# Kernel tuning notes

Measured on AMD Instinct MI355X. Metric: run time of the kernel, lower is better.

The kernel has to match this reference:

```python
import jax, jax.numpy as jnp
import numpy as np

N_NODES = 100000


def gcn_conv(x, edge_index, W, b):
    """PyG GCNConv: add self-loops, symmetric deg^{-1/2} normalization,
    linear transform, scatter-add aggregation, then bias."""
    n = x.shape[0]
    loops = jnp.arange(n, dtype=edge_index.dtype)
    src = jnp.concatenate([edge_index[0], loops])  # [E+N]
    dst = jnp.concatenate([edge_index[1], loops])  # [E+N]
    # degree (with self-loops) of each target node
    deg = jax.ops.segment_sum(jnp.ones_like(dst, dtype=x.dtype), dst, num_segments=n)
    dinv = jnp.where(deg > 0, jax.lax.rsqrt(deg), 0.0)
    norm = dinv[src] * dinv[dst]  # [E+N]
    h = x @ W  # [N, out_dim] -- transform before aggregation
    msg = h[src] * norm[:, None]  # gather + normalize
    out = jax.ops.segment_sum(msg, dst, num_segments=n)  # scatter-add
    return out + b


def setup_inputs() -> dict:
    key = jax.random.key(0)
    ks = jax.random.split(key, 8)
    n, e, d_in, d_h = N_NODES, 1600000, 32, 64
    x = jax.random.normal(ks[0], (n, d_in), dtype=jnp.float32)
    edge_index = jax.random.randint(ks[1], (2, e), 0, n, dtype=jnp.int64)
    # Glorot-style init for GCN weights, uniform for linear layer
    W1 = jax.random.normal(ks[2], (d_in, d_h), dtype=jnp.float32) / np.sqrt(d_in)
    b1 = jnp.zeros((d_h,), dtype=jnp.float32)
    W2 = jax.random.normal(ks[3], (d_h, d_h), dtype=jnp.float32) / np.sqrt(d_h)
    b2 = jnp.zeros((d_h,), dtype=jnp.float32)
    Wo = jax.random.normal(ks[4], (d_h, 1), dtype=jnp.float32) / np.sqrt(d_h)
    bo = jnp.zeros((1,), dtype=jnp.float32)
    return {"x": x, "edge_index": edge_index, "W1": W1, "b1": b1,
            "W2": W2, "b2": b2, "Wo": Wo, "bo": bo}


def reference(x, edge_index, W1, b1, W2, b2, Wo, bo):
    h = jax.nn.relu(gcn_conv(x, edge_index, W1, b1))
    h = jax.nn.relu(gcn_conv(h, edge_index, W2, b2))
    logits = h @ Wo + bo  # [N, 1]
    return jax.nn.sigmoid(logits).squeeze(-1)  # [N]
```

## Files before the change

### kernel.cpp

```cpp
#include <hip/hip_runtime.h>

#define DH 64
#define DIN 32
#define BSH 8
#define BNODES 256
#define MAXB 1024
#define CAPSH 13
#define CAP (1 << CAPSH)

typedef unsigned short u16;
typedef unsigned int u32;
typedef float f32x2 __attribute__((ext_vector_type(2)));

__device__ __forceinline__ float bf2f(u16 u) {
    union { u32 i; float f; } x; x.i = ((u32)u) << 16; return x.f;
}
__device__ __forceinline__ u16 f2bf(float f) {
    union { float f; u32 i; } x; x.f = f;
    u32 r = x.i + 0x7fff + ((x.i >> 16) & 1);
    return (u16)(r >> 16);
}
__device__ __forceinline__ float bfl(u32 u) {
    union { u32 i; float f; } x; x.i = u << 16; return x.f;
}
__device__ __forceinline__ float bfh(u32 u) {
    union { u32 i; float f; } x; x.i = u & 0xffff0000u; return x.f;
}
__device__ __forceinline__ void pkacc(f32x2& a, u32 u) {
    f32x2 b;
    b[0] = bfl(u); b[1] = bfh(u);
    asm("v_pk_add_f32 %0, %1, %0" : "+v"(a) : "v"(b));
}

__global__ void __launch_bounds__(256) binA_k(
        const int* __restrict__ ei, int* __restrict__ gcnt,
        u32* __restrict__ pairs, int E, int n, int nbuck) {
    __shared__ int lhist[MAXB];
    __shared__ int lbase[MAXB];
    __shared__ int smode;
    int t = threadIdx.x;
    if (t < 64) {
        int v = (2 * t + 1 < 2 * E) ? ei[2 * t + 1] : 0;
        unsigned long long b = __ballot(v != 0);
        if (t == 0) smode = (b != 0ULL) ? 1 : 0;
    }
    for (int b = t; b < nbuck; b += 256) lhist[b] = 0;
    __syncthreads();
    int m = smode;
    unsigned un = (unsigned)n;
    int q0 = blockIdx.x * 256 + t;
    int qs = gridDim.x * 256;

    if (m && !(E & 3)) {
        const int4* d4 = (const int4*)(ei + E);
        for (int q = q0; q < (E >> 2); q += qs) {
            int4 d = d4[q];
            if ((unsigned)d.x < un) atomicAdd(&lhist[d.x >> BSH], 1);
            if ((unsigned)d.y < un) atomicAdd(&lhist[d.y >> BSH], 1);
            if ((unsigned)d.z < un) atomicAdd(&lhist[d.z >> BSH], 1);
            if ((unsigned)d.w < un) atomicAdd(&lhist[d.w >> BSH], 1);
        }
    } else if (!m && !(E & 1)) {
        const int4* d4 = (const int4*)(ei + 2 * E);
        for (int q = q0; q < (E >> 1); q += qs) {
            int4 d = d4[q];
            if ((unsigned)d.x < un) atomicAdd(&lhist[d.x >> BSH], 1);
            if ((unsigned)d.z < un) atomicAdd(&lhist[d.z >> BSH], 1);
        }
    } else {
        const int* dstp = m ? (ei + E) : (ei + 2 * E);
        int stride = m ? 1 : 2;
        for (int e = q0; e < E; e += qs) {
            int d = dstp[(size_t)e * stride];
            if ((unsigned)d < un) atomicAdd(&lhist[d >> BSH], 1);
        }
    }
    __syncthreads();
    for (int b = t; b < nbuck; b += 256) {
        int c = lhist[b];
        lbase[b] = c ? ((b << CAPSH) + atomicAdd(&gcnt[b], c)) : 0;
        lhist[b] = 0;
    }
    __syncthreads();
    #define EMIT(S, D)                                                     \
        if ((unsigned)(D) < un) {                                          \
            int sv = ((unsigned)(S) < un) ? (S) : 0;                       \
            int bb = (D) >> BSH;                                           \
            int off = atomicAdd(&lhist[bb], 1);                            \
            int pos = lbase[bb] + off;                                     \
            if (pos < ((bb + 1) << CAPSH))                                 \
                pairs[pos] = ((u32)sv << BSH) | (u32)((D) & (BNODES - 1)); \
        }
    if (m && !(E & 3)) {
        const int4* s4 = (const int4*)ei;
        const int4* d4 = (const int4*)(ei + E);
        for (int q = q0; q < (E >> 2); q += qs) {
            int4 s = s4[q]; int4 d = d4[q];
            EMIT(s.x, d.x) EMIT(s.y, d.y) EMIT(s.z, d.z) EMIT(s.w, d.w)
        }
    } else if (!m && !(E & 1)) {
        const int4* s4 = (const int4*)ei;
        const int4* d4 = (const int4*)(ei + 2 * E);
        for (int q = q0; q < (E >> 1); q += qs) {
            int4 s = s4[q]; int4 d = d4[q];
            EMIT(s.x, d.x) EMIT(s.z, d.z)
        }
    } else {
        const int* srcp = ei;
        const int* dstp = m ? (ei + E) : (ei + 2 * E);
        int stride = m ? 1 : 2;
        for (int e = q0; e < E; e += qs) {
            int d = dstp[(size_t)e * stride];
            int s = srcp[(size_t)e * stride];
            EMIT(s, d)
        }
    }
    #undef EMIT
}

__global__ void __launch_bounds__(512) csr_build_k(
        const u32* __restrict__ pairs, const int* __restrict__ gcnt,
        int* __restrict__ rstart, int* __restrict__ rend,
        int* __restrict__ col, float* __restrict__ dinv, int N) {
    __shared__ int cnt[BNODES];
    __shared__ int s[BNODES];
    int b = blockIdx.x, t = threadIdx.x;
    int base = b << CAPSH;
    int ec = gcnt[b]; if (ec > CAP) ec = CAP;
    int end = base + ec;
    if (t < BNODES) cnt[t] = 0;
    __syncthreads();
    for (int i = base + t; i < end; i += 512)
        atomicAdd(&cnt[pairs[i] & (BNODES - 1)], 1);
    __syncthreads();
    int v = (t < BNODES) ? cnt[t] : 0;
    if (t < BNODES) s[t] = v;
    __syncthreads();
    for (int off = 1; off < BNODES; off <<= 1) {
        int xsc = (t >= off && t < BNODES) ? s[t - off] : 0;
        __syncthreads();
        if (t < BNODES) s[t] += xsc;
        __syncthreads();
    }
    if (t < BNODES) {
        int excl = s[t] - v;
        int a = base + excl;
        int node = (b << BSH) + t;
        if (node < N) {
            rstart[node] = a;
            rend[node]   = a + v;
            dinv[node]   = rsqrtf((float)v + 1.0f);
        }
        cnt[t] = a;
    }
    __syncthreads();
    for (int i = base + t; i < end; i += 512) {
        u32 p = pairs[i];
        int pos = atomicAdd(&cnt[p & (BNODES - 1)], 1);
        col[pos] = (int)(p >> BSH);
    }
}

__global__ void __launch_bounds__(256) gemm1_k(
        const float* __restrict__ x, const float* __restrict__ W1,
        const float* __restrict__ dinv, u16* __restrict__ hp, int N) {
    __shared__ float Wl[DIN * DH];
    __shared__ float xl[16][DIN + 4];
    int t = threadIdx.x;
    {
        const float4* Wv = (const float4*)W1;
        float4* Wd = (float4*)Wl;
        #pragma unroll
        for (int r = 0; r < 2; r++) Wd[t + 256 * r] = Wv[t + 256 * r];
    }
    if (blockIdx.x == 0 && t < 32)
        ((float*)(hp + (size_t)N * DH))[t] = 0.f;
    if (t < 128) {
        int row = t >> 3, ck = (t & 7) * 4;
        int node = blockIdx.x * 16 + row;
        float4 vx = {0.f, 0.f, 0.f, 0.f};
        if (node < N)
            vx = *(const float4*)&x[(size_t)node * DIN + ck];
        *(float4*)&xl[row][ck] = vx;
    }
    __syncthreads();
    int lane = t & 63, w = t >> 6;
    int g = lane >> 4, c = lane & 15;
    int nl = w * 4 + g;
    int node = blockIdx.x * 16 + nl;
    const float* xr = xl[nl];
    float4 acc = {0.f, 0.f, 0.f, 0.f};
    #pragma unroll
    for (int k = 0; k < DIN; k++) {
        float xv = xr[k];
        float4 wv = *(const float4*)&Wl[k * DH + c * 4];
        acc.x += xv * wv.x; acc.y += xv * wv.y; acc.z += xv * wv.z; acc.w += xv * wv.w;
    }
    if (node < N) {
        float di = dinv[node];
        ushort4 o;
        o.x = f2bf(acc.x * di); o.y = f2bf(acc.y * di);
        o.z = f2bf(acc.z * di); o.w = f2bf(acc.w * di);
        *(ushort4*)&hp[(size_t)node * DH + c * 4] = o;
    }
}

__device__ __forceinline__ void edge_sum8_db(const u16* __restrict__ hp,
                                             const int* __restrict__ col,
                                             int start, int deg, int g, int c,
                                             int nsent, f32x2* __restrict__ acc) {
    int dm = deg;
    dm = max(dm, __shfl_xor(dm, 8, 64));
    dm = max(dm, __shfl_xor(dm, 16, 64));
    dm = max(dm, __shfl_xor(dm, 32, 64));
    if (dm <= 0) return;
    int gl = g << 3;
    u32 co = (u32)c << 4;
    const char* hpb = (const char*)hp;
    #define COLS(B) (((B) < dm && (B) + c < deg) ? col[start + (B) + c] : nsent)
    #define ISSUE(V, CB)                                                     \
        { _Pragma("unroll") for (int j = 0; j < 8; j++) {                    \
              int s_ = __shfl((CB), gl | j, 64);                             \
              (V)[j] = *(const uint4*)(hpb + ((((u32)s_) << 7) | co)); } }
    #define ACCUM(V)                                                         \
        { _Pragma("unroll") for (int j = 0; j < 8; j++) {                    \
              pkacc(acc[0], (V)[j].x); pkacc(acc[1], (V)[j].y);              \
              pkacc(acc[2], (V)[j].z); pkacc(acc[3], (V)[j].w); } }
    uint4 va[8], vb[8];
    int cbA = COLS(0);
    ISSUE(va, cbA)
    int cbB = COLS(8);
    for (int base = 0; base < dm; base += 16) {
        bool hb = base + 8 < dm;
        if (hb) ISSUE(vb, cbB)
        int cbN1 = COLS(base + 16);
        ACCUM(va)
        if (base + 16 < dm) ISSUE(va, cbN1)
        int cbN2 = COLS(base + 24);
        if (hb) ACCUM(vb)
        cbB = cbN2;
    }
    #undef COLS
    #undef ISSUE
    #undef ACCUM
}

__global__ void __launch_bounds__(256) agg_gemm_k(
        const u16* __restrict__ hp, const int* __restrict__ rstart,
        const int* __restrict__ rend, const int* __restrict__ col,
        const float* __restrict__ dinv, const float* __restrict__ b1,
        const float* __restrict__ W2, u16* __restrict__ hp2, int N) {
    __shared__ float Wl[DH * DH];
    __shared__ float xs[4][8][DH + 4];
    int tid = threadIdx.x;
    {
        const float4* Wv = (const float4*)W2;
        float4* Wd = (float4*)Wl;
        #pragma unroll
        for (int r = 0; r < 4; r++) Wd[tid + 256 * r] = Wv[tid + 256 * r];
    }
    if (blockIdx.x == 0 && tid < 32)
        ((float*)(hp2 + (size_t)N * DH))[tid] = 0.f;
    __syncthreads();
    int lane = tid & 63, w = tid >> 6;
    int g = lane >> 3, c = lane & 7;
    int node = blockIdx.x * 32 + w * 8 + g;
    int start = 0, deg = 0;
    if (node < N) { start = rstart[node]; deg = rend[node] - start; }
    f32x2 acc[4] = {{0.f,0.f},{0.f,0.f},{0.f,0.f},{0.f,0.f}};
    edge_sum8_db(hp, col, start, deg, g, c, N, acc);
    float di = (node < N) ? dinv[node] : 0.f;
    float o0=0.f,o1=0.f,o2=0.f,o3=0.f,o4=0.f,o5=0.f,o6=0.f,o7=0.f;
    if (node < N) {
        uint4 sv = *(const uint4*)&hp[(size_t)node * DH + c * 8];
        float4 blo = *(const float4*)&b1[c * 8];
        float4 bhi = *(const float4*)&b1[c * 8 + 4];
        o0 = fmaxf((acc[0][0] + bfl(sv.x)) * di + blo.x, 0.f);
        o1 = fmaxf((acc[0][1] + bfh(sv.x)) * di + blo.y, 0.f);
        o2 = fmaxf((acc[1][0] + bfl(sv.y)) * di + blo.z, 0.f);
        o3 = fmaxf((acc[1][1] + bfh(sv.y)) * di + blo.w, 0.f);
        o4 = fmaxf((acc[2][0] + bfl(sv.z)) * di + bhi.x, 0.f);
        o5 = fmaxf((acc[2][1] + bfh(sv.z)) * di + bhi.y, 0.f);
        o6 = fmaxf((acc[3][0] + bfl(sv.w)) * di + bhi.z, 0.f);
        o7 = fmaxf((acc[3][1] + bfh(sv.w)) * di + bhi.w, 0.f);
    }
    *(float4*)&xs[w][g][c * 8]     = make_float4(o0, o1, o2, o3);
    *(float4*)&xs[w][g][c * 8 + 4] = make_float4(o4, o5, o6, o7);
    const float* xr = xs[w][g];
    float4 alo = {0.f,0.f,0.f,0.f}, ahi = {0.f,0.f,0.f,0.f};
    #pragma unroll
    for (int k4 = 0; k4 < DH / 4; k4++) {
        float4 xv4 = *(const float4*)&xr[k4 * 4];
        float xj[4] = {xv4.x, xv4.y, xv4.z, xv4.w};
        #pragma unroll
        for (int j = 0; j < 4; j++) {
            const float* wr = &Wl[(k4 * 4 + j) * DH + c * 8];
            float4 w0 = *(const float4*)wr;
            float4 w1 = *(const float4*)(wr + 4);
            float xv = xj[j];
            alo.x += xv * w0.x; alo.y += xv * w0.y; alo.z += xv * w0.z; alo.w += xv * w0.w;
            ahi.x += xv * w1.x; ahi.y += xv * w1.y; ahi.z += xv * w1.z; ahi.w += xv * w1.w;
        }
    }
    if (node < N) {
        uint4 po;
        po.x = (u32)f2bf(alo.x * di) | ((u32)f2bf(alo.y * di) << 16);
        po.y = (u32)f2bf(alo.z * di) | ((u32)f2bf(alo.w * di) << 16);
        po.z = (u32)f2bf(ahi.x * di) | ((u32)f2bf(ahi.y * di) << 16);
        po.w = (u32)f2bf(ahi.z * di) | ((u32)f2bf(ahi.w * di) << 16);
        *(uint4*)&hp2[(size_t)node * DH + c * 8] = po;
    }
}

__global__ void __launch_bounds__(256) agg_head_k(
        const u16* __restrict__ hp, const int* __restrict__ rstart,
        const int* __restrict__ rend, const int* __restrict__ col,
        const float* __restrict__ dinv, const float* __restrict__ bias,
        const float* __restrict__ Wo, const float* __restrict__ bo,
        float* __restrict__ y, int N) {
    int lane = threadIdx.x & 63;
    int g = lane >> 3, c = lane & 7;
    int node = blockIdx.x * 32 + (threadIdx.x >> 6) * 8 + g;
    int start = 0, deg = 0;
    if (node < N) { start = rstart[node]; deg = rend[node] - start; }
    f32x2 acc[4] = {{0.f,0.f},{0.f,0.f},{0.f,0.f},{0.f,0.f}};
    edge_sum8_db(hp, col, start, deg, g, c, N, acc);
    float t = 0.f;
    if (node < N) {
        uint4 sv = *(const uint4*)&hp[(size_t)node * DH + c * 8];
        float4 blo = *(const float4*)&bias[c * 8];
        float4 bhi = *(const float4*)&bias[c * 8 + 4];
        float4 wlo = *(const float4*)&Wo[c * 8];
        float4 whi = *(const float4*)&Wo[c * 8 + 4];
        float di = dinv[node];
        t = fmaxf((acc[0][0] + bfl(sv.x)) * di + blo.x, 0.f) * wlo.x
          + fmaxf((acc[0][1] + bfh(sv.x)) * di + blo.y, 0.f) * wlo.y
          + fmaxf((acc[1][0] + bfl(sv.y)) * di + blo.z, 0.f) * wlo.z
          + fmaxf((acc[1][1] + bfh(sv.y)) * di + blo.w, 0.f) * wlo.w
          + fmaxf((acc[2][0] + bfl(sv.z)) * di + bhi.x, 0.f) * whi.x
          + fmaxf((acc[2][1] + bfh(sv.z)) * di + bhi.y, 0.f) * whi.y
          + fmaxf((acc[3][0] + bfl(sv.w)) * di + bhi.z, 0.f) * whi.z
          + fmaxf((acc[3][1] + bfh(sv.w)) * di + bhi.w, 0.f) * whi.w;
    }
    t += __shfl_xor(t, 1, 64);
    t += __shfl_xor(t, 2, 64);
    t += __shfl_xor(t, 4, 64);
    if (c == 0 && node < N) {
        float z = t + bo[0];
        y[node] = 1.f / (1.f + __expf(-z));
    }
}

extern "C" void kernel_launch(void* const* d_in, const int* in_sizes, int n_in,
                              void* d_out, int out_size, void* d_ws, size_t ws_size,
                              hipStream_t stream) {
    const float* x  = (const float*)d_in[0];
    const int*   ei = (const int*)d_in[1];
    const float* W1 = (const float*)d_in[2];
    const float* b1 = (const float*)d_in[3];
    const float* W2 = (const float*)d_in[4];
    const float* b2 = (const float*)d_in[5];
    const float* Wo = (const float*)d_in[6];
    const float* bo = (const float*)d_in[7];
    float* y = (float*)d_out;

    int N = in_sizes[0] / DIN;
    int E = in_sizes[1] / 2;
    int nbuck = ((N - 1) >> BSH) + 1;

    char* ws = (char*)d_ws;
    size_t off = 0;
    auto alloc = [&](size_t bytes) { char* p = ws + off; off += (bytes + 255) & ~(size_t)255; return p; };
    int*   gcnt   = (int*)alloc(MAXB * 4);
    int*   rstart = (int*)alloc((size_t)N * 4);
    int*   rend   = (int*)alloc((size_t)N * 4);
    float* dinv   = (float*)alloc((size_t)N * 4);
    int*   col    = (int*)alloc(((size_t)nbuck << CAPSH) * 4);
    size_t pair_b = ((size_t)nbuck << CAPSH) * 4;
    size_t hp_b   = (size_t)N * DH * 2 + 256;
    char*  bufA   = (char*)alloc(pair_b > hp_b ? pair_b : hp_b);
    u16*   bufB   = (u16*)alloc(hp_b);
    u16*   hp    = (u16*)bufA;
    u32*   pairs = (u32*)bufA;

    hipMemsetAsync(gcnt, 0, (size_t)nbuck * 4, stream);
    binA_k<<<256, 256, 0, stream>>>(ei, gcnt, pairs, E, N, nbuck);
    csr_build_k<<<nbuck, 512, 0, stream>>>(pairs, gcnt, rstart, rend, col, dinv, N);
    gemm1_k<<<(N + 15) / 16, 256, 0, stream>>>(x, W1, dinv, hp, N);
    agg_gemm_k<<<(N + 31) / 32, 256, 0, stream>>>(hp, rstart, rend, col, dinv, b1, W2, bufB, N);
    agg_head_k<<<(N + 31) / 32, 256, 0, stream>>>(bufB, rstart, rend, col, dinv, b2, Wo, bo, y, N);
}
```

Before: 195.6 us.

## Use rolling gather pipeline, pre-shifted column offsets, shuffle-based GEMM, larger binning blocks

The double-buffered 16-wide gather in the aggregation kernels is replaced by a rolling 8-register pipeline that overlaps each load with accumulation, which cuts register pressure. Occupancy hints of 8 blocks per CU are added. Column indices are now stored as byte offsets (index shifted left by 7), so the gather no longer shifts. The second-layer GEMM broadcasts activations with wave shuffles instead of staging them in shared memory. The binning kernel runs 512 threads per block. Smaller in-flight load depth may reduce memory-level parallelism per wave, and the shifted offsets limit node counts to what fits in 32 bits.

```diff
diff --git a/kernel.cpp b/kernel.cpp
--- a/kernel.cpp
+++ b/kernel.cpp
@@ -32,7 +32,7 @@
     asm("v_pk_add_f32 %0, %1, %0" : "+v"(a) : "v"(b));
 }
 
-__global__ void __launch_bounds__(256) binA_k(
+__global__ void __launch_bounds__(512) binA_k(
         const int* __restrict__ ei, int* __restrict__ gcnt,
         u32* __restrict__ pairs, int E, int n, int nbuck) {
     __shared__ int lhist[MAXB];
@@ -44,12 +44,12 @@
         unsigned long long b = __ballot(v != 0);
         if (t == 0) smode = (b != 0ULL) ? 1 : 0;
     }
-    for (int b = t; b < nbuck; b += 256) lhist[b] = 0;
+    for (int b = t; b < nbuck; b += 512) lhist[b] = 0;
     __syncthreads();
     int m = smode;
     unsigned un = (unsigned)n;
-    int q0 = blockIdx.x * 256 + t;
-    int qs = gridDim.x * 256;
+    int q0 = blockIdx.x * 512 + t;
+    int qs = gridDim.x * 512;
 
     if (m && !(E & 3)) {
         const int4* d4 = (const int4*)(ei + E);
@@ -76,7 +76,7 @@
         }
     }
     __syncthreads();
-    for (int b = t; b < nbuck; b += 256) {
+    for (int b = t; b < nbuck; b += 512) {
         int c = lhist[b];
         lbase[b] = c ? ((b << CAPSH) + atomicAdd(&gcnt[b], c)) : 0;
         lhist[b] = 0;
@@ -157,7 +157,7 @@
     for (int i = base + t; i < end; i += 512) {
         u32 p = pairs[i];
         int pos = atomicAdd(&cnt[p & (BNODES - 1)], 1);
-        col[pos] = (int)(p >> BSH);
+        col[pos] = (int)((p >> BSH) << 7);
     }
 }
 
@@ -205,53 +205,77 @@
     }
 }
 
-__device__ __forceinline__ void edge_sum8_db(const u16* __restrict__ hp,
-                                             const int* __restrict__ col,
-                                             int start, int deg, int g, int c,
-                                             int nsent, f32x2* __restrict__ acc) {
+__device__ __forceinline__ void edge_sum_roll8(const u16* __restrict__ hp,
+                                               const int* __restrict__ colb,
+                                               int start, int deg, int gl, int c,
+                                               int sentb, f32x2* __restrict__ acc) {
     int dm = deg;
     dm = max(dm, __shfl_xor(dm, 8, 64));
     dm = max(dm, __shfl_xor(dm, 16, 64));
     dm = max(dm, __shfl_xor(dm, 32, 64));
     if (dm <= 0) return;
-    int gl = g << 3;
-    u32 co = (u32)c << 4;
-    const char* hpb = (const char*)hp;
-    #define COLS(B) (((B) < dm && (B) + c < deg) ? col[start + (B) + c] : nsent)
-    #define ISSUE(V, CB)                                                     \
-        { _Pragma("unroll") for (int j = 0; j < 8; j++) {                    \
-              int s_ = __shfl((CB), gl | j, 64);                             \
-              (V)[j] = *(const uint4*)(hpb + ((((u32)s_) << 7) | co)); } }
-    #define ACCUM(V)                                                         \
-        { _Pragma("unroll") for (int j = 0; j < 8; j++) {                    \
-              pkacc(acc[0], (V)[j].x); pkacc(acc[1], (V)[j].y);              \
-              pkacc(acc[2], (V)[j].z); pkacc(acc[3], (V)[j].w); } }
-    uint4 va[8], vb[8];
-    int cbA = COLS(0);
-    ISSUE(va, cbA)
-    int cbB = COLS(8);
-    for (int base = 0; base < dm; base += 16) {
-        bool hb = base + 8 < dm;
-        if (hb) ISSUE(vb, cbB)
-        int cbN1 = COLS(base + 16);
-        ACCUM(va)
-        if (base + 16 < dm) ISSUE(va, cbN1)
-        int cbN2 = COLS(base + 24);
-        if (hb) ACCUM(vb)
-        cbB = cbN2;
-    }
-    #undef COLS
-    #undef ISSUE
-    #undef ACCUM
-}
-
-__global__ void __launch_bounds__(256) agg_gemm_k(
+    const char* hpco = (const char*)hp + ((u32)c << 4);
+    int nch = (dm + 7) >> 3;
+    uint4 v0, v1, v2, v3, v4, v5, v6, v7;
+    int cb = (c < deg) ? colb[start + c] : sentb;
+    {
+        int s;
+        s = __shfl(cb, gl | 0, 64); v0 = *(const uint4*)(hpco + s);
+        s = __shfl(cb, gl | 1, 64); v1 = *(const uint4*)(hpco + s);
+        s = __shfl(cb, gl | 2, 64); v2 = *(const uint4*)(hpco + s);
+        s = __shfl(cb, gl | 3, 64); v3 = *(const uint4*)(hpco + s);
+        s = __shfl(cb, gl | 4, 64); v4 = *(const uint4*)(hpco + s);
+        s = __shfl(cb, gl | 5, 64); v5 = *(const uint4*)(hpco + s);
+        s = __shfl(cb, gl | 6, 64); v6 = *(const uint4*)(hpco + s);
+        s = __shfl(cb, gl | 7, 64); v7 = *(const uint4*)(hpco + s);
+    }
+    int cbn = (8 + c < deg) ? colb[start + 8 + c] : sentb;
+    for (int ch = 1; ch < nch; ch++) {
+        int cbu = cbn;
+        int nb2 = (ch + 1) << 3;
+        cbn = (nb2 + c < deg) ? colb[start + nb2 + c] : sentb;
+        int s;
+        s = __shfl(cbu, gl | 0, 64);
+        pkacc(acc[0], v0.x); pkacc(acc[1], v0.y); pkacc(acc[2], v0.z); pkacc(acc[3], v0.w);
+        v0 = *(const uint4*)(hpco + s);
+        s = __shfl(cbu, gl | 1, 64);
+        pkacc(acc[0], v1.x); pkacc(acc[1], v1.y); pkacc(acc[2], v1.z); pkacc(acc[3], v1.w);
+        v1 = *(const uint4*)(hpco + s);
+        s = __shfl(cbu, gl | 2, 64);
+        pkacc(acc[0], v2.x); pkacc(acc[1], v2.y); pkacc(acc[2], v2.z); pkacc(acc[3], v2.w);
+        v2 = *(const uint4*)(hpco + s);
+        s = __shfl(cbu, gl | 3, 64);
+        pkacc(acc[0], v3.x); pkacc(acc[1], v3.y); pkacc(acc[2], v3.z); pkacc(acc[3], v3.w);
+        v3 = *(const uint4*)(hpco + s);
+        s = __shfl(cbu, gl | 4, 64);
+        pkacc(acc[0], v4.x); pkacc(acc[1], v4.y); pkacc(acc[2], v4.z); pkacc(acc[3], v4.w);
+        v4 = *(const uint4*)(hpco + s);
+        s = __shfl(cbu, gl | 5, 64);
+        pkacc(acc[0], v5.x); pkacc(acc[1], v5.y); pkacc(acc[2], v5.z); pkacc(acc[3], v5.w);
+        v5 = *(const uint4*)(hpco + s);
+        s = __shfl(cbu, gl | 6, 64);
+        pkacc(acc[0], v6.x); pkacc(acc[1], v6.y); pkacc(acc[2], v6.z); pkacc(acc[3], v6.w);
+        v6 = *(const uint4*)(hpco + s);
+        s = __shfl(cbu, gl | 7, 64);
+        pkacc(acc[0], v7.x); pkacc(acc[1], v7.y); pkacc(acc[2], v7.z); pkacc(acc[3], v7.w);
+        v7 = *(const uint4*)(hpco + s);
+    }
+    pkacc(acc[0], v0.x); pkacc(acc[1], v0.y); pkacc(acc[2], v0.z); pkacc(acc[3], v0.w);
+    pkacc(acc[0], v1.x); pkacc(acc[1], v1.y); pkacc(acc[2], v1.z); pkacc(acc[3], v1.w);
+    pkacc(acc[0], v2.x); pkacc(acc[1], v2.y); pkacc(acc[2], v2.z); pkacc(acc[3], v2.w);
+    pkacc(acc[0], v3.x); pkacc(acc[1], v3.y); pkacc(acc[2], v3.z); pkacc(acc[3], v3.w);
+    pkacc(acc[0], v4.x); pkacc(acc[1], v4.y); pkacc(acc[2], v4.z); pkacc(acc[3], v4.w);
+    pkacc(acc[0], v5.x); pkacc(acc[1], v5.y); pkacc(acc[2], v5.z); pkacc(acc[3], v5.w);
+    pkacc(acc[0], v6.x); pkacc(acc[1], v6.y); pkacc(acc[2], v6.z); pkacc(acc[3], v6.w);
+    pkacc(acc[0], v7.x); pkacc(acc[1], v7.y); pkacc(acc[2], v7.z); pkacc(acc[3], v7.w);
+}
+
+__global__ void __launch_bounds__(256, 8) agg_gemm_k(
         const u16* __restrict__ hp, const int* __restrict__ rstart,
         const int* __restrict__ rend, const int* __restrict__ col,
         const float* __restrict__ dinv, const float* __restrict__ b1,
         const float* __restrict__ W2, u16* __restrict__ hp2, int N) {
     __shared__ float Wl[DH * DH];
-    __shared__ float xs[4][8][DH + 4];
     int tid = threadIdx.x;
     {
         const float4* Wv = (const float4*)W2;
@@ -262,13 +286,13 @@
     if (blockIdx.x == 0 && tid < 32)
         ((float*)(hp2 + (size_t)N * DH))[tid] = 0.f;
     __syncthreads();
-    int lane = tid & 63, w = tid >> 6;
-    int g = lane >> 3, c = lane & 7;
-    int node = blockIdx.x * 32 + w * 8 + g;
+    int lane = tid & 63;
+    int g = lane >> 3, c = lane & 7, gl = g << 3;
+    int node = blockIdx.x * 32 + (tid >> 6) * 8 + g;
     int start = 0, deg = 0;
     if (node < N) { start = rstart[node]; deg = rend[node] - start; }
     f32x2 acc[4] = {{0.f,0.f},{0.f,0.f},{0.f,0.f},{0.f,0.f}};
-    edge_sum8_db(hp, col, start, deg, g, c, N, acc);
+    edge_sum_roll8(hp, col, start, deg, gl, c, N << 7, acc);
     float di = (node < N) ? dinv[node] : 0.f;
     float o0=0.f,o1=0.f,o2=0.f,o3=0.f,o4=0.f,o5=0.f,o6=0.f,o7=0.f;
     if (node < N) {
@@ -284,20 +308,25 @@
         o6 = fmaxf((acc[3][0] + bfl(sv.w)) * di + bhi.z, 0.f);
         o7 = fmaxf((acc[3][1] + bfh(sv.w)) * di + bhi.w, 0.f);
     }
-    *(float4*)&xs[w][g][c * 8]     = make_float4(o0, o1, o2, o3);
-    *(float4*)&xs[w][g][c * 8 + 4] = make_float4(o4, o5, o6, o7);
-    const float* xr = xs[w][g];
     float4 alo = {0.f,0.f,0.f,0.f}, ahi = {0.f,0.f,0.f,0.f};
     #pragma unroll
-    for (int k4 = 0; k4 < DH / 4; k4++) {
-        float4 xv4 = *(const float4*)&xr[k4 * 4];
-        float xj[4] = {xv4.x, xv4.y, xv4.z, xv4.w};
+    for (int kk = 0; kk < 8; kk++) {
+        int sl = gl + kk;
+        float x0 = __shfl(o0, sl, 64);
+        float x1 = __shfl(o1, sl, 64);
+        float x2 = __shfl(o2, sl, 64);
+        float x3 = __shfl(o3, sl, 64);
+        float x4 = __shfl(o4, sl, 64);
+        float x5 = __shfl(o5, sl, 64);
+        float x6 = __shfl(o6, sl, 64);
+        float x7 = __shfl(o7, sl, 64);
+        float xm[8] = {x0, x1, x2, x3, x4, x5, x6, x7};
         #pragma unroll
-        for (int j = 0; j < 4; j++) {
-            const float* wr = &Wl[(k4 * 4 + j) * DH + c * 8];
+        for (int m = 0; m < 8; m++) {
+            const float* wr = &Wl[(kk * 8 + m) * DH + c * 8];
             float4 w0 = *(const float4*)wr;
             float4 w1 = *(const float4*)(wr + 4);
-            float xv = xj[j];
+            float xv = xm[m];
             alo.x += xv * w0.x; alo.y += xv * w0.y; alo.z += xv * w0.z; alo.w += xv * w0.w;
             ahi.x += xv * w1.x; ahi.y += xv * w1.y; ahi.z += xv * w1.z; ahi.w += xv * w1.w;
         }
@@ -312,19 +341,19 @@
     }
 }
 
-__global__ void __launch_bounds__(256) agg_head_k(
+__global__ void __launch_bounds__(256, 8) agg_head_k(
         const u16* __restrict__ hp, const int* __restrict__ rstart,
         const int* __restrict__ rend, const int* __restrict__ col,
         const float* __restrict__ dinv, const float* __restrict__ bias,
         const float* __restrict__ Wo, const float* __restrict__ bo,
         float* __restrict__ y, int N) {
     int lane = threadIdx.x & 63;
-    int g = lane >> 3, c = lane & 7;
+    int g = lane >> 3, c = lane & 7, gl = g << 3;
     int node = blockIdx.x * 32 + (threadIdx.x >> 6) * 8 + g;
     int start = 0, deg = 0;
     if (node < N) { start = rstart[node]; deg = rend[node] - start; }
     f32x2 acc[4] = {{0.f,0.f},{0.f,0.f},{0.f,0.f},{0.f,0.f}};
-    edge_sum8_db(hp, col, start, deg, g, c, N, acc);
+    edge_sum_roll8(hp, col, start, deg, gl, c, N << 7, acc);
     float t = 0.f;
     if (node < N) {
         uint4 sv = *(const uint4*)&hp[(size_t)node * DH + c * 8];
@@ -384,7 +413,7 @@
     u32*   pairs = (u32*)bufA;
 
     hipMemsetAsync(gcnt, 0, (size_t)nbuck * 4, stream);
-    binA_k<<<256, 256, 0, stream>>>(ei, gcnt, pairs, E, N, nbuck);
+    binA_k<<<256, 512, 0, stream>>>(ei, gcnt, pairs, E, N, nbuck);
     csr_build_k<<<nbuck, 512, 0, stream>>>(pairs, gcnt, rstart, rend, col, dinv, N);
     gemm1_k<<<(N + 15) / 16, 256, 0, stream>>>(x, W1, dinv, hp, N);
     agg_gemm_k<<<(N + 31) / 32, 256, 0, stream>>>(hp, rstart, rend, col, dinv, b1, W2, bufB, N);
```

Result: slower. 588.0 us (+200.7%).

## Pack row ranges, prescale column byte offsets, and widen binning blocks

Applied to the files above, without the earlier changes.

Row start and end are stored together as an int2, so each node reads one 8-byte word instead of two separate loads. Column indices are stored already shifted into byte offsets (times 128), which removes the shift and OR from the gather address math in the aggregation loop. The binning kernel now uses 512-thread blocks on the same 256-block grid. Storing prescaled 32-bit offsets limits N to about 16M nodes, and the larger blocks raise shared-atomic contention per block.

```diff
diff --git a/kernel.cpp b/kernel.cpp
--- a/kernel.cpp
+++ b/kernel.cpp
@@ -32,7 +32,7 @@
     asm("v_pk_add_f32 %0, %1, %0" : "+v"(a) : "v"(b));
 }
 
-__global__ void __launch_bounds__(256) binA_k(
+__global__ void __launch_bounds__(512) binA_k(
         const int* __restrict__ ei, int* __restrict__ gcnt,
         u32* __restrict__ pairs, int E, int n, int nbuck) {
     __shared__ int lhist[MAXB];
@@ -44,12 +44,12 @@
         unsigned long long b = __ballot(v != 0);
         if (t == 0) smode = (b != 0ULL) ? 1 : 0;
     }
-    for (int b = t; b < nbuck; b += 256) lhist[b] = 0;
+    for (int b = t; b < nbuck; b += 512) lhist[b] = 0;
     __syncthreads();
     int m = smode;
     unsigned un = (unsigned)n;
-    int q0 = blockIdx.x * 256 + t;
-    int qs = gridDim.x * 256;
+    int q0 = blockIdx.x * 512 + t;
+    int qs = gridDim.x * 512;
 
     if (m && !(E & 3)) {
         const int4* d4 = (const int4*)(ei + E);
@@ -76,7 +76,7 @@
         }
     }
     __syncthreads();
-    for (int b = t; b < nbuck; b += 256) {
+    for (int b = t; b < nbuck; b += 512) {
         int c = lhist[b];
         lbase[b] = c ? ((b << CAPSH) + atomicAdd(&gcnt[b], c)) : 0;
         lhist[b] = 0;
@@ -120,7 +120,7 @@
 
 __global__ void __launch_bounds__(512) csr_build_k(
         const u32* __restrict__ pairs, const int* __restrict__ gcnt,
-        int* __restrict__ rstart, int* __restrict__ rend,
+        int2* __restrict__ rse,
         int* __restrict__ col, float* __restrict__ dinv, int N) {
     __shared__ int cnt[BNODES];
     __shared__ int s[BNODES];
@@ -147,9 +147,8 @@
         int a = base + excl;
         int node = (b << BSH) + t;
         if (node < N) {
-            rstart[node] = a;
-            rend[node]   = a + v;
-            dinv[node]   = rsqrtf((float)v + 1.0f);
+            rse[node]  = make_int2(a, a + v);
+            dinv[node] = rsqrtf((float)v + 1.0f);
         }
         cnt[t] = a;
     }
@@ -157,7 +156,7 @@
     for (int i = base + t; i < end; i += 512) {
         u32 p = pairs[i];
         int pos = atomicAdd(&cnt[p & (BNODES - 1)], 1);
-        col[pos] = (int)(p >> BSH);
+        col[pos] = (int)((p >> BSH) << 7);
     }
 }
 
@@ -206,22 +205,20 @@
 }
 
 __device__ __forceinline__ void edge_sum8_db(const u16* __restrict__ hp,
-                                             const int* __restrict__ col,
-                                             int start, int deg, int g, int c,
-                                             int nsent, f32x2* __restrict__ acc) {
+                                             const int* __restrict__ colb,
+                                             int start, int deg, int gl, int c,
+                                             int sentb, f32x2* __restrict__ acc) {
     int dm = deg;
     dm = max(dm, __shfl_xor(dm, 8, 64));
     dm = max(dm, __shfl_xor(dm, 16, 64));
     dm = max(dm, __shfl_xor(dm, 32, 64));
     if (dm <= 0) return;
-    int gl = g << 3;
-    u32 co = (u32)c << 4;
-    const char* hpb = (const char*)hp;
-    #define COLS(B) (((B) < dm && (B) + c < deg) ? col[start + (B) + c] : nsent)
+    const char* hpco = (const char*)hp + ((u32)c << 4);
+    #define COLS(B) (((B) < dm && (B) + c < deg) ? colb[start + (B) + c] : sentb)
     #define ISSUE(V, CB)                                                     \
         { _Pragma("unroll") for (int j = 0; j < 8; j++) {                    \
               int s_ = __shfl((CB), gl | j, 64);                             \
-              (V)[j] = *(const uint4*)(hpb + ((((u32)s_) << 7) | co)); } }
+              (V)[j] = *(const uint4*)(hpco + s_); } }
     #define ACCUM(V)                                                         \
         { _Pragma("unroll") for (int j = 0; j < 8; j++) {                    \
               pkacc(acc[0], (V)[j].x); pkacc(acc[1], (V)[j].y);              \
@@ -246,8 +243,8 @@
 }
 
 __global__ void __launch_bounds__(256) agg_gemm_k(
-        const u16* __restrict__ hp, const int* __restrict__ rstart,
-        const int* __restrict__ rend, const int* __restrict__ col,
+        const u16* __restrict__ hp, const int2* __restrict__ rse,
+        const int* __restrict__ col,
         const float* __restrict__ dinv, const float* __restrict__ b1,
         const float* __restrict__ W2, u16* __restrict__ hp2, int N) {
     __shared__ float Wl[DH * DH];
@@ -263,12 +260,12 @@
         ((float*)(hp2 + (size_t)N * DH))[tid] = 0.f;
     __syncthreads();
     int lane = tid & 63, w = tid >> 6;
-    int g = lane >> 3, c = lane & 7;
+    int g = lane >> 3, c = lane & 7, gl = g << 3;
     int node = blockIdx.x * 32 + w * 8 + g;
     int start = 0, deg = 0;
-    if (node < N) { start = rstart[node]; deg = rend[node] - start; }
+    if (node < N) { int2 se = rse[node]; start = se.x; deg = se.y - se.x; }
     f32x2 acc[4] = {{0.f,0.f},{0.f,0.f},{0.f,0.f},{0.f,0.f}};
-    edge_sum8_db(hp, col, start, deg, g, c, N, acc);
+    edge_sum8_db(hp, col, start, deg, gl, c, N << 7, acc);
     float di = (node < N) ? dinv[node] : 0.f;
     float o0=0.f,o1=0.f,o2=0.f,o3=0.f,o4=0.f,o5=0.f,o6=0.f,o7=0.f;
     if (node < N) {
@@ -313,18 +310,18 @@
 }
 
 __global__ void __launch_bounds__(256) agg_head_k(
-        const u16* __restrict__ hp, const int* __restrict__ rstart,
-        const int* __restrict__ rend, const int* __restrict__ col,
+        const u16* __restrict__ hp, const int2* __restrict__ rse,
+        const int* __restrict__ col,
         const float* __restrict__ dinv, const float* __restrict__ bias,
         const float* __restrict__ Wo, const float* __restrict__ bo,
         float* __restrict__ y, int N) {
     int lane = threadIdx.x & 63;
-    int g = lane >> 3, c = lane & 7;
+    int g = lane >> 3, c = lane & 7, gl = g << 3;
     int node = blockIdx.x * 32 + (threadIdx.x >> 6) * 8 + g;
     int start = 0, deg = 0;
-    if (node < N) { start = rstart[node]; deg = rend[node] - start; }
+    if (node < N) { int2 se = rse[node]; start = se.x; deg = se.y - se.x; }
     f32x2 acc[4] = {{0.f,0.f},{0.f,0.f},{0.f,0.f},{0.f,0.f}};
-    edge_sum8_db(hp, col, start, deg, g, c, N, acc);
+    edge_sum8_db(hp, col, start, deg, gl, c, N << 7, acc);
     float t = 0.f;
     if (node < N) {
         uint4 sv = *(const uint4*)&hp[(size_t)node * DH + c * 8];
@@ -372,8 +369,7 @@
     size_t off = 0;
     auto alloc = [&](size_t bytes) { char* p = ws + off; off += (bytes + 255) & ~(size_t)255; return p; };
     int*   gcnt   = (int*)alloc(MAXB * 4);
-    int*   rstart = (int*)alloc((size_t)N * 4);
-    int*   rend   = (int*)alloc((size_t)N * 4);
+    int2*  rse    = (int2*)alloc((size_t)N * 8);
     float* dinv   = (float*)alloc((size_t)N * 4);
     int*   col    = (int*)alloc(((size_t)nbuck << CAPSH) * 4);
     size_t pair_b = ((size_t)nbuck << CAPSH) * 4;
@@ -384,9 +380,9 @@
     u32*   pairs = (u32*)bufA;
 
     hipMemsetAsync(gcnt, 0, (size_t)nbuck * 4, stream);
-    binA_k<<<256, 256, 0, stream>>>(ei, gcnt, pairs, E, N, nbuck);
-    csr_build_k<<<nbuck, 512, 0, stream>>>(pairs, gcnt, rstart, rend, col, dinv, N);
+    binA_k<<<256, 512, 0, stream>>>(ei, gcnt, pairs, E, N, nbuck);
+    csr_build_k<<<nbuck, 512, 0, stream>>>(pairs, gcnt, rse, col, dinv, N);
     gemm1_k<<<(N + 15) / 16, 256, 0, stream>>>(x, W1, dinv, hp, N);
-    agg_gemm_k<<<(N + 31) / 32, 256, 0, stream>>>(hp, rstart, rend, col, dinv, b1, W2, bufB, N);
-    agg_head_k<<<(N + 31) / 32, 256, 0, stream>>>(bufB, rstart, rend, col, dinv, b2, Wo, bo, y, N);
-}
+    agg_gemm_k<<<(N + 31) / 32, 256, 0, stream>>>(hp, rse, col, dinv, b1, W2, bufB, N);
+    agg_head_k<<<(N + 31) / 32, 256, 0, stream>>>(bufB, rse, col, dinv, b2, Wo, bo, y, N);
+}
```

New measurement: 191.8 us. No clear change (-1.9%).
